# Kernel tuning notes

Hardware: AMD Instinct MI355X
Metric: run time of the kernel (lower is better)

## Reference

```python
import jax, jax.numpy as jnp
import numpy as np

B, T, H = 128, 1024, 200
IN0, OUT = 8, 4  # GRU layer-0 input size (4 targets + 4 emotion), fc output dim


def setup_inputs() -> dict:
    key = jax.random.key(0)
    ks = jax.random.split(key, 12)
    s = 1.0 / np.sqrt(H)  # torch RNN default init: U(-1/sqrt(H), 1/sqrt(H))
    u = lambda k, shp: jax.random.uniform(k, shp, jnp.float32, -s, s)
    return {
        "x": jax.random.normal(ks[0], (B, T, IN0), jnp.float32),
        "W_ih0": u(ks[1], (3 * H, IN0)),
        "W_hh0": u(ks[2], (3 * H, H)),
        "b_ih0": u(ks[3], (3 * H,)),
        "b_hh0": u(ks[4], (3 * H,)),
        "W_ih1": u(ks[5], (3 * H, H)),
        "W_hh1": u(ks[6], (3 * H, H)),
        "b_ih1": u(ks[7], (3 * H,)),
        "b_hh1": u(ks[8], (3 * H,)),
        "W_fc": u(ks[9], (OUT, H)),
        "b_fc": u(ks[10], (OUT,)),
        "xlens": jax.random.randint(ks[11], (B,), 1, T + 1),
    }


def _gru_cell(h, gx, W_hh, b_hh):
    # torch GRU cell: gx = W_ih @ x + b_ih precomputed, gates order [r, z, n]
    gh = h @ W_hh.T + b_hh
    ir, iz, i_n = jnp.split(gx, 3, axis=-1)
    hr, hz, hn = jnp.split(gh, 3, axis=-1)
    r = jax.nn.sigmoid(ir + hr)
    z = jax.nn.sigmoid(iz + hz)
    n = jnp.tanh(i_n + r * hn)
    return (1.0 - z) * n + z * h


def _forward(x, W_ih0, W_hh0, b_ih0, b_hh0, W_ih1, W_hh1, b_ih1, b_hh1, W_fc, b_fc):
    b, t, _ = x.shape
    emotion = x[:, 0, -4:]                      # (B,4) frozen at t=0, as in source
    targets = x[:, :, :4]                       # (B,T,4)
    # step inputs: t=0 -> ones(B,4); t>0 -> targets[:, t-1] (teacher forcing)
    tf = jnp.concatenate([jnp.ones((b, 1, 4), x.dtype), targets[:, :-1, :]], axis=1)
    inputs = jnp.concatenate(
        [tf, jnp.broadcast_to(emotion[:, None, :], (b, t, 4))], axis=-1)  # (B,T,8)
    # precompute layer-0 input projections for all steps (one big GEMM)
    gx0 = jnp.einsum("btc,gc->btg", inputs, W_ih0) + b_ih0  # (B,T,3H)

    def step(carry, gx0_t):
        h0, h1 = carry
        h0 = _gru_cell(h0, gx0_t, W_hh0, b_hh0)
        gx1 = h0 @ W_ih1.T + b_ih1
        h1 = _gru_cell(h1, gx1, W_hh1, b_hh1)
        out = jnp.tanh(h1 @ W_fc.T + b_fc)      # fused fc + tanh
        return (h0, h1), out

    h0 = jnp.zeros((b, H), x.dtype)
    h1 = jnp.zeros((b, H), x.dtype)
    _, outs = jax.lax.scan(step, (h0, h1), jnp.swapaxes(gx0, 0, 1))  # (T,B,4)
    return jnp.swapaxes(outs, 0, 1)             # (B,T,4)


def reference(x, W_ih0, W_hh0, b_ih0, b_hh0, W_ih1, W_hh1, b_ih1, b_hh1, W_fc, b_fc, xlens):
    # xlens is accepted but unused, exactly as in the source forward()
    return _forward(x, W_ih0, W_hh0, b_ih0, b_hh0, W_ih1, W_hh1, b_ih1, b_hh1, W_fc, b_fc)
```

## Files before the change

kernel.cpp:

```cpp
#include <hip/hip_runtime.h>
#include <hip/hip_bf16.h>


#define TT 1024
#define HH 200
#define NB 16
#define HS 13
#define KP 232

typedef __attribute__((ext_vector_type(8))) short short8;
typedef __attribute__((ext_vector_type(4))) float f32x4;

__device__ __forceinline__ float sigm(float v) { return 1.0f / (1.0f + __expf(-v)); }
__device__ __forceinline__ float tanh_fast(float v) {
  float e = __expf(-2.0f * v);
  return (1.0f - e) / (1.0f + e);
}
__device__ __forceinline__ uint llc_load_u32(const uint* p) {
  return __hip_atomic_load(p, __ATOMIC_RELAXED, __HIP_MEMORY_SCOPE_SYSTEM);
}
__device__ __forceinline__ void llc_store_u32(uint* p, uint v) {
  __hip_atomic_store(p, v, __ATOMIC_RELAXED, __HIP_MEMORY_SCOPE_SYSTEM);
}
__device__ __forceinline__ float bfu2f(ushort u) {
  return __uint_as_float(((uint)u) << 16);
}
__device__ __forceinline__ ushort f2bfu(float f) {
  __hip_bfloat16 b = __float2bfloat16(f);
  return *(ushort*)&b;
}
__device__ __forceinline__ uint packf(float h) {
  ushort hi = f2bfu(h);
  float  fh = bfu2f(hi);
  ushort lo = f2bfu(h - fh);
  return (uint)hi | ((uint)lo << 16);
}

__global__ __launch_bounds__(256, 1) void gru2_mfma(
    const float* __restrict__ x,
    const float* __restrict__ Wih0, const float* __restrict__ Whh0,
    const float* __restrict__ bih0, const float* __restrict__ bhh0,
    const float* __restrict__ Wih1, const float* __restrict__ Whh1,
    const float* __restrict__ bih1, const float* __restrict__ bhh1,
    const float* __restrict__ Wfc,  const float* __restrict__ bfc,
    float* __restrict__ out,
    uint* __restrict__ h0g, uint* __restrict__ h1g, int* __restrict__ bars)
{
  __shared__ __align__(16) ushort hBh[2][NB][KP];
  __shared__ __align__(16) ushort hBl[2][NB][KP];
  __shared__ float D[117][17];
  __shared__ float Wi0[39][8];
  __shared__ float bi0[39], bh0[39], bi1[39], bh1[39], bfs[4];
  __shared__ float xc[NB][8];

  const int tid  = threadIdx.x;
  const int wave = tid >> 6;
  const int lane = tid & 63;
  const int m15  = lane & 15;
  const int q    = lane >> 4;

  const int g  = blockIdx.x & 7;
  const int s  = blockIdx.x >> 3;
  const int b0 = g * NB;
  const int j0 = s * HS;
  const int hs = (HH - j0 < HS) ? (HH - j0) : HS;
  const int th   = 3 * hs;
  const int h0r  = 6 * hs;
  const int T0   = (h0r + 15) >> 4;
  const int NT   = T0 + ((th + 15) >> 4);
  const bool isOut = (s == 15);

  short8 Ah[2][7], Al[2][7];
  #pragma unroll
  for (int mt = 0; mt < 2; ++mt) {
    const int T = wave * 2 + mt;
    const bool fc  = isOut && (wave == 2) && (mt == 0);
    const bool val = fc || (T < NT);
    #pragma unroll
    for (int kt = 0; kt < 7; ++kt) {
      short8 vh = {0,0,0,0,0,0,0,0}, vl = {0,0,0,0,0,0,0,0};
      #pragma unroll
      for (int j = 0; j < 8; ++j) {
        const int k = kt * 32 + q * 8 + j;
        float w = 0.0f;
        if (val && k < HH) {
          if (fc) {
            if (m15 < 4) w = Wfc[m15 * HH + k];
          } else {
            const int p = T * 16 + m15;
            int r = -1;
            if (p < h0r) r = p;
            else if (p >= T0 * 16 && (p - T0 * 16) < th) r = h0r + (p - T0 * 16);
            if (r >= 0) {
              const int m  = r / th, rr = r - m * th;
              const int qq = rr / hs, jj = rr - qq * hs;
              const float* src = (m == 0) ? Whh0 : ((m == 1) ? Wih1 : Whh1);
              w = src[(qq * HH + j0 + jj) * HH + k];
            }
          }
        }
        const ushort uh = f2bfu(w);
        const ushort ul = f2bfu(w - bfu2f(uh));
        vh[j] = (short)uh; vl[j] = (short)ul;
      }
      Ah[mt][kt] = vh; Al[mt][kt] = vl;
    }
  }

  for (int u = tid; u < th * 8; u += 256) {
    int rr = u >> 3, c = u & 7;
    int qq = rr / hs, jj = rr - qq * hs;
    Wi0[rr][c] = Wih0[(qq * HH + j0 + jj) * 8 + c];
  }
  for (int u = tid; u < th; u += 256) {
    int qq = u / hs, jj = u - qq * hs;
    int grow = qq * HH + j0 + jj;
    bi0[u] = bih0[grow]; bh0[u] = bhh0[grow];
    bi1[u] = bih1[grow]; bh1[u] = bhh1[grow];
  }
  if (tid < 4) bfs[tid] = bfc[tid];
  for (int u = tid; u < 2 * NB * KP / 2; u += 256) ((uint*)hBh)[u] = 0;
  for (int u = tid; u < 2 * NB * KP / 2; u += 256) ((uint*)hBl)[u] = 0;
  __syncthreads();

  int* bar = &bars[g * 64];
  const int cj = tid >> 4, cb = tid & 15;

  for (int t = 0; t <= TT + 1; ++t) {
    const uint* h0src = h0g + ((t + 1) & 1) * (128 * HH);
    const uint* h1src = h1g + (t & 1) * (128 * HH);
    uint tmp[25];
    #pragma unroll
    for (int i = 0; i < 25; ++i) {
      const int u  = tid + i * 256;
      const int st = u / 3200, rem = u - st * 3200;
      const int b  = rem / 200, k = rem - b * 200;
      tmp[i] = llc_load_u32(&(st ? h1src : h0src)[(b0 + b) * HH + k]);
    }
    #pragma unroll
    for (int i = 0; i < 25; ++i) {
      const int u  = tid + i * 256;
      const int st = u / 3200, rem = u - st * 3200;
      const int b  = rem / 200, k = rem - b * 200;
      hBh[st][b][k] = (ushort)(tmp[i] & 0xffff);
      hBl[st][b][k] = (ushort)(tmp[i] >> 16);
    }
    if (tid < 128 && t < TT) {
      int b = tid >> 3, c = tid & 7;
      float v;
      if (c < 4) v = (t == 0) ? 1.0f : x[((b0 + b) * TT + (t - 1)) * 8 + c];
      else       v = x[(b0 + b) * TT * 8 + c];
      xc[b][c] = v;
    }
    __syncthreads();

    #pragma unroll
    for (int mt = 0; mt < 2; ++mt) {
      const int T = wave * 2 + mt;
      const bool fc  = isOut && (wave == 2) && (mt == 0);
      const bool val = fc || (T < NT);
      if (!val) continue;
      const int st = fc ? 1 : ((T < T0) ? 0 : 1);
      const ushort* Bh = &hBh[st][m15][0];
      const ushort* Bl = &hBl[st][m15][0];
      f32x4 acc = {0.f, 0.f, 0.f, 0.f};
      #pragma unroll
      for (int kt = 0; kt < 7; ++kt) {
        const short8 bh = *(const short8*)&Bh[kt * 32 + q * 8];
        const short8 bl = *(const short8*)&Bl[kt * 32 + q * 8];
        acc = __builtin_amdgcn_mfma_f32_16x16x32_bf16(Ah[mt][kt], bh, acc, 0, 0, 0);
        acc = __builtin_amdgcn_mfma_f32_16x16x32_bf16(Ah[mt][kt], bl, acc, 0, 0, 0);
        acc = __builtin_amdgcn_mfma_f32_16x16x32_bf16(Al[mt][kt], bh, acc, 0, 0, 0);
      }
      if (fc) {
        if (t >= 2) {
          #pragma unroll
          for (int i = 0; i < 4; ++i) {
            const int p = q * 4 + i;
            if (p < 4)
              out[((b0 + m15) * TT + (t - 2)) * 4 + p] = tanh_fast(acc[i] + bfs[p]);
          }
        }
      } else {
        #pragma unroll
        for (int i = 0; i < 4; ++i) {
          const int p = T * 16 + q * 4 + i;
          int r = -1;
          if (p < h0r) r = p;
          else if (p >= T0 * 16 && (p - T0 * 16) < th) r = h0r + (p - T0 * 16);
          if (r >= 0) D[r][m15] = acc[i];
        }
      }
    }
    __syncthreads();

    if (cj < hs) {
      const float hv0 = bfu2f(hBh[0][cb][j0 + cj]) + bfu2f(hBl[0][cb][j0 + cj]);
      const float hv1 = bfu2f(hBh[1][cb][j0 + cj]) + bfu2f(hBl[1][cb][j0 + cj]);
      if (t < TT) {
        float ir = bi0[cj], iz = bi0[hs + cj], in_ = bi0[2 * hs + cj];
        #pragma unroll
        for (int c = 0; c < 8; ++c) {
          const float xv = xc[cb][c];
          ir  += Wi0[cj][c] * xv;
          iz  += Wi0[hs + cj][c] * xv;
          in_ += Wi0[2 * hs + cj][c] * xv;
        }
        const float hr = D[cj][cb] + bh0[cj];
        const float hz = D[hs + cj][cb] + bh0[hs + cj];
        const float hn = D[2 * hs + cj][cb] + bh0[2 * hs + cj];
        const float r = sigm(ir + hr), z = sigm(iz + hz);
        const float n = tanh_fast(in_ + r * hn);
        llc_store_u32(&h0g[(t & 1) * (128 * HH) + (b0 + cb) * HH + j0 + cj],
                      packf((1.0f - z) * n + z * hv0));
      }
      if (t >= 1 && t <= TT) {
        const float ir  = D[3 * hs + cj][cb] + bi1[cj];
        const float iz  = D[4 * hs + cj][cb] + bi1[hs + cj];
        const float in_ = D[5 * hs + cj][cb] + bi1[2 * hs + cj];
        const float hr  = D[6 * hs + cj][cb] + bh1[cj];
        const float hz  = D[7 * hs + cj][cb] + bh1[hs + cj];
        const float hn  = D[8 * hs + cj][cb] + bh1[2 * hs + cj];
        const float r = sigm(ir + hr), z = sigm(iz + hz);
        const float n = tanh_fast(in_ + r * hn);
        llc_store_u32(&h1g[((t + 1) & 1) * (128 * HH) + (b0 + cb) * HH + j0 + cj],
                      packf((1.0f - z) * n + z * hv1));
      }
    }

    __syncthreads();
    if (tid == 0) {
      __hip_atomic_fetch_add(bar, 1, __ATOMIC_RELAXED, __HIP_MEMORY_SCOPE_SYSTEM);
      const int target = 16 * (t + 1);
      while (__hip_atomic_load(bar, __ATOMIC_RELAXED, __HIP_MEMORY_SCOPE_SYSTEM) < target)
        __builtin_amdgcn_s_sleep(1);
    }
    __syncthreads();
  }
}

extern "C" void kernel_launch(void* const* d_in, const int* in_sizes, int n_in,
                              void* d_out, int out_size, void* d_ws, size_t ws_size,
                              hipStream_t stream) {
  uint* ws = (uint*)d_ws;
  hipMemsetAsync(d_ws, 0, (size_t)(102400 + 512) * sizeof(uint), stream);
  gru2_mfma<<<128, 256, 0, stream>>>(
      (const float*)d_in[0],
      (const float*)d_in[1], (const float*)d_in[2],
      (const float*)d_in[3], (const float*)d_in[4],
      (const float*)d_in[5], (const float*)d_in[6],
      (const float*)d_in[7], (const float*)d_in[8],
      (const float*)d_in[9], (const float*)d_in[10],
      (float*)d_out, ws, ws + 51200, (int*)(ws + 102400));
}
```

Measured before the change: 3.170 ms.

## Replace atomic counter barrier with per-block flags and MFMA-fragment LDS layout

The shared atomic counter barrier (one fetch_add plus spin per block per step) is replaced by per-block step flags. Each block writes its own flag and wave 0 polls all 16 flags in its group with a wave vote. The hidden-state staging in LDS is changed to a fragment-major layout so each lane reads its MFMA B operand with one contiguous 16-byte load per k-tile. Both tiles of a wave now share the same B loads. This aims to cut barrier contention and LDS read overhead on the serial recurrence, at the cost of relying on relaxed flag ordering for correctness.

```diff
diff --git a/kernel.cpp b/kernel.cpp
--- a/kernel.cpp
+++ b/kernel.cpp
@@ -2,11 +2,12 @@
 #include <hip/hip_bf16.h>
 
 
-#define TT 1024
-#define HH 200
-#define NB 16
-#define HS 13
-#define KP 232
+#define TT   1024
+#define HH   200
+#define NB   16
+#define HS   13
+#define HBUF 25600
+#define PST  3584
 
 typedef __attribute__((ext_vector_type(8))) short short8;
 typedef __attribute__((ext_vector_type(4))) float f32x4;
@@ -22,21 +23,18 @@
 __device__ __forceinline__ void llc_store_u32(uint* p, uint v) {
   __hip_atomic_store(p, v, __ATOMIC_RELAXED, __HIP_MEMORY_SCOPE_SYSTEM);
 }
-__device__ __forceinline__ float bfu2f(ushort u) {
-  return __uint_as_float(((uint)u) << 16);
-}
+__device__ __forceinline__ float bfu2f(ushort u) { return __uint_as_float(((uint)u) << 16); }
 __device__ __forceinline__ ushort f2bfu(float f) {
   __hip_bfloat16 b = __float2bfloat16(f);
   return *(ushort*)&b;
 }
 __device__ __forceinline__ uint packf(float h) {
   ushort hi = f2bfu(h);
-  float  fh = bfu2f(hi);
-  ushort lo = f2bfu(h - fh);
-  return (uint)hi | ((uint)lo << 16);
-}
-
-__global__ __launch_bounds__(256, 1) void gru2_mfma(
+  ushort lo = f2bfu(h - bfu2f(hi));
+  return (uint)hi | (((uint)lo) << 16);
+}
+
+__global__ __launch_bounds__(256, 1) void gru2_frag(
     const float* __restrict__ x,
     const float* __restrict__ Wih0, const float* __restrict__ Whh0,
     const float* __restrict__ bih0, const float* __restrict__ bhh0,
@@ -44,10 +42,10 @@
     const float* __restrict__ bih1, const float* __restrict__ bhh1,
     const float* __restrict__ Wfc,  const float* __restrict__ bfc,
     float* __restrict__ out,
-    uint* __restrict__ h0g, uint* __restrict__ h1g, int* __restrict__ bars)
+    uint* __restrict__ h0g, uint* __restrict__ h1g, uint* __restrict__ flags)
 {
-  __shared__ __align__(16) ushort hBh[2][NB][KP];
-  __shared__ __align__(16) ushort hBl[2][NB][KP];
+  __shared__ __align__(16) ushort hFh[2 * PST];
+  __shared__ __align__(16) ushort hFl[2 * PST];
   __shared__ float D[117][17];
   __shared__ float Wi0[39][8];
   __shared__ float bi0[39], bh0[39], bi1[39], bh1[39], bfs[4];
@@ -64,139 +62,188 @@
   const int b0 = g * NB;
   const int j0 = s * HS;
   const int hs = (HH - j0 < HS) ? (HH - j0) : HS;
-  const int th   = 3 * hs;
-  const int h0r  = 6 * hs;
-  const int T0   = (h0r + 15) >> 4;
-  const int NT   = T0 + ((th + 15) >> 4);
+  const int th  = 3 * hs;
+  const int h0r = 6 * hs;
+  const int T0  = (h0r + 15) >> 4;
+  const int NT  = T0 + ((th + 15) >> 4);
   const bool isOut = (s == 15);
 
   short8 Ah[2][7], Al[2][7];
   #pragma unroll
-  for (int mt = 0; mt < 2; ++mt) {
-    const int T = wave * 2 + mt;
-    const bool fc  = isOut && (wave == 2) && (mt == 0);
-    const bool val = fc || (T < NT);
+  for (int tt = 0; tt < 2; ++tt) {
+    const int T = 2 * wave + tt;
+    const bool isFC = isOut && (T == NT);
+    const bool val  = (T < NT) || isFC;
     #pragma unroll
     for (int kt = 0; kt < 7; ++kt) {
       short8 vh = {0,0,0,0,0,0,0,0}, vl = {0,0,0,0,0,0,0,0};
-      #pragma unroll
-      for (int j = 0; j < 8; ++j) {
-        const int k = kt * 32 + q * 8 + j;
-        float w = 0.0f;
-        if (val && k < HH) {
-          if (fc) {
-            if (m15 < 4) w = Wfc[m15 * HH + k];
-          } else {
-            const int p = T * 16 + m15;
-            int r = -1;
-            if (p < h0r) r = p;
-            else if (p >= T0 * 16 && (p - T0 * 16) < th) r = h0r + (p - T0 * 16);
-            if (r >= 0) {
-              const int m  = r / th, rr = r - m * th;
-              const int qq = rr / hs, jj = rr - qq * hs;
-              const float* src = (m == 0) ? Whh0 : ((m == 1) ? Wih1 : Whh1);
-              w = src[(qq * HH + j0 + jj) * HH + k];
+      if (val) {
+        #pragma unroll
+        for (int j = 0; j < 8; ++j) {
+          const int k = kt * 32 + q * 8 + j;
+          float w = 0.0f;
+          if (k < HH) {
+            if (isFC) {
+              if (m15 < 4) w = Wfc[m15 * HH + k];
+            } else {
+              const int p = T * 16 + m15;
+              int r = -1;
+              if (p < h0r) r = p;
+              else { const int pp = p - T0 * 16; if (pp >= 0 && pp < th) r = h0r + pp; }
+              if (r >= 0) {
+                const int m = r / th, rr = r - m * th;
+                const int q3 = rr / hs, jj = rr - q3 * hs;
+                const float* src = (m == 0) ? Whh0 : ((m == 1) ? Wih1 : Whh1);
+                w = src[(q3 * HH + j0 + jj) * HH + k];
+              }
             }
           }
-        }
-        const ushort uh = f2bfu(w);
-        const ushort ul = f2bfu(w - bfu2f(uh));
-        vh[j] = (short)uh; vl[j] = (short)ul;
-      }
-      Ah[mt][kt] = vh; Al[mt][kt] = vl;
-    }
-  }
-
+          const ushort hi = f2bfu(w);
+          const ushort lo = f2bfu(w - bfu2f(hi));
+          vh[j] = (short)hi; vl[j] = (short)lo;
+        }
+      }
+      Ah[tt][kt] = vh; Al[tt][kt] = vl;
+    }
+  }
+
+  for (int u = tid; u < 2 * PST; u += 256) { hFh[u] = 0; hFl[u] = 0; }
   for (int u = tid; u < th * 8; u += 256) {
-    int rr = u >> 3, c = u & 7;
-    int qq = rr / hs, jj = rr - qq * hs;
-    Wi0[rr][c] = Wih0[(qq * HH + j0 + jj) * 8 + c];
+    const int rr = u >> 3, c = u & 7;
+    const int q3 = rr / hs, jj = rr - q3 * hs;
+    Wi0[rr][c] = Wih0[(q3 * HH + j0 + jj) * 8 + c];
   }
   for (int u = tid; u < th; u += 256) {
-    int qq = u / hs, jj = u - qq * hs;
-    int grow = qq * HH + j0 + jj;
+    const int q3 = u / hs, jj = u - q3 * hs;
+    const int grow = q3 * HH + j0 + jj;
     bi0[u] = bih0[grow]; bh0[u] = bhh0[grow];
     bi1[u] = bih1[grow]; bh1[u] = bhh1[grow];
   }
   if (tid < 4) bfs[tid] = bfc[tid];
-  for (int u = tid; u < 2 * NB * KP / 2; u += 256) ((uint*)hBh)[u] = 0;
-  for (int u = tid; u < 2 * NB * KP / 2; u += 256) ((uint*)hBl)[u] = 0;
+
+  int boff[25], lofs[25]; uint stm = 0;
+  #pragma unroll
+  for (int i = 0; i < 25; ++i) {
+    const int u  = tid + i * 256;
+    const int b  = u & 15;
+    const int v2 = u >> 4;
+    const int st = (v2 >= 200) ? 1 : 0;
+    const int k  = v2 - st * 200;
+    const int kt = k >> 5, r32 = k & 31, qq = r32 >> 3, j = r32 & 7;
+    boff[i] = (b0 + b) * HH + k;
+    lofs[i] = st * PST + kt * 512 + (b + 16 * qq) * 8 + j;
+    if (st) stm |= (1u << i);
+  }
+
+  const int cj = tid >> 4, cb = tid & 15;
+  const bool gAct = (cj < hs);
+  int hvix = 0;
+  if (gAct) {
+    const int k = j0 + cj;
+    const int kt = k >> 5, r32 = k & 31, qq = r32 >> 3, j = r32 & 7;
+    hvix = kt * 512 + (cb + 16 * qq) * 8 + j;
+  }
+
+  uint* const flg = flags + g * 32;
   __syncthreads();
 
-  int* bar = &bars[g * 64];
-  const int cj = tid >> 4, cb = tid & 15;
-
   for (int t = 0; t <= TT + 1; ++t) {
-    const uint* h0src = h0g + ((t + 1) & 1) * (128 * HH);
-    const uint* h1src = h1g + (t & 1) * (128 * HH);
-    uint tmp[25];
-    #pragma unroll
-    for (int i = 0; i < 25; ++i) {
-      const int u  = tid + i * 256;
-      const int st = u / 3200, rem = u - st * 3200;
-      const int b  = rem / 200, k = rem - b * 200;
-      tmp[i] = llc_load_u32(&(st ? h1src : h0src)[(b0 + b) * HH + k]);
-    }
-    #pragma unroll
-    for (int i = 0; i < 25; ++i) {
-      const int u  = tid + i * 256;
-      const int st = u / 3200, rem = u - st * 3200;
-      const int b  = rem / 200, k = rem - b * 200;
-      hBh[st][b][k] = (ushort)(tmp[i] & 0xffff);
-      hBl[st][b][k] = (ushort)(tmp[i] >> 16);
-    }
     if (tid < 128 && t < TT) {
-      int b = tid >> 3, c = tid & 7;
+      const int b = tid >> 3, c = tid & 7;
       float v;
       if (c < 4) v = (t == 0) ? 1.0f : x[((b0 + b) * TT + (t - 1)) * 8 + c];
       else       v = x[(b0 + b) * TT * 8 + c];
       xc[b][c] = v;
     }
-    __syncthreads();
-
+
+    if (wave == 0) {
+      const uint tgt = (uint)t;
+      for (;;) {
+        const uint f = (lane < 16) ? llc_load_u32(flg + lane) : tgt;
+        if (__all((int)(f >= tgt))) break;
+        __builtin_amdgcn_s_sleep(2);
+      }
+    }
+    __syncthreads();
+
+    const uint* h0s = h0g + ((t + 1) & 1) * HBUF;
+    const uint* h1s = h1g + (t & 1) * HBUF;
+    uint v[25];
     #pragma unroll
-    for (int mt = 0; mt < 2; ++mt) {
-      const int T = wave * 2 + mt;
-      const bool fc  = isOut && (wave == 2) && (mt == 0);
-      const bool val = fc || (T < NT);
-      if (!val) continue;
-      const int st = fc ? 1 : ((T < T0) ? 0 : 1);
-      const ushort* Bh = &hBh[st][m15][0];
-      const ushort* Bl = &hBl[st][m15][0];
-      f32x4 acc = {0.f, 0.f, 0.f, 0.f};
+    for (int i = 0; i < 25; ++i)
+      v[i] = llc_load_u32((((stm >> i) & 1) ? h1s : h0s) + boff[i]);
+    #pragma unroll
+    for (int i = 0; i < 25; ++i) {
+      hFh[lofs[i]] = (ushort)(v[i] & 0xffffu);
+      hFl[lofs[i]] = (ushort)(v[i] >> 16);
+    }
+    __syncthreads();
+
+    {
+      const int  Ta = 2 * wave, Tb = Ta + 1;
+      const bool fa = isOut && (Ta == NT);
+      const bool fb = isOut && (Tb == NT);
+      const bool va = (Ta < NT) || fa, vb = (Tb < NT) || fb;
+      const int  sa = (fa || Ta >= T0) ? 1 : 0;
+      const int  sb = (fb || Tb >= T0) ? 1 : 0;
+      f32x4 acc0 = {0.f,0.f,0.f,0.f}, acc1 = {0.f,0.f,0.f,0.f};
+      const int lb = lane * 8;
       #pragma unroll
-      for (int kt = 0; kt < 7; ++kt) {
-        const short8 bh = *(const short8*)&Bh[kt * 32 + q * 8];
-        const short8 bl = *(const short8*)&Bl[kt * 32 + q * 8];
-        acc = __builtin_amdgcn_mfma_f32_16x16x32_bf16(Ah[mt][kt], bh, acc, 0, 0, 0);
-        acc = __builtin_amdgcn_mfma_f32_16x16x32_bf16(Ah[mt][kt], bl, acc, 0, 0, 0);
-        acc = __builtin_amdgcn_mfma_f32_16x16x32_bf16(Al[mt][kt], bh, acc, 0, 0, 0);
-      }
-      if (fc) {
-        if (t >= 2) {
-          #pragma unroll
-          for (int i = 0; i < 4; ++i) {
-            const int p = q * 4 + i;
-            if (p < 4)
-              out[((b0 + m15) * TT + (t - 2)) * 4 + p] = tanh_fast(acc[i] + bfs[p]);
+      for (int st = 0; st < 2; ++st) {
+        const bool nA = va && (sa == st), nB = vb && (sb == st);
+        if (!(nA || nB)) continue;
+        const ushort* bh = hFh + st * PST + lb;
+        const ushort* bl = hFl + st * PST + lb;
+        #pragma unroll
+        for (int kt = 0; kt < 7; ++kt) {
+          const short8 Bh = *(const short8*)(bh + kt * 512);
+          const short8 Bl = *(const short8*)(bl + kt * 512);
+          if (nA) {
+            acc0 = __builtin_amdgcn_mfma_f32_16x16x32_bf16(Ah[0][kt], Bh, acc0, 0, 0, 0);
+            acc0 = __builtin_amdgcn_mfma_f32_16x16x32_bf16(Ah[0][kt], Bl, acc0, 0, 0, 0);
+            acc0 = __builtin_amdgcn_mfma_f32_16x16x32_bf16(Al[0][kt], Bh, acc0, 0, 0, 0);
           }
-        }
-      } else {
+          if (nB) {
+            acc1 = __builtin_amdgcn_mfma_f32_16x16x32_bf16(Ah[1][kt], Bh, acc1, 0, 0, 0);
+            acc1 = __builtin_amdgcn_mfma_f32_16x16x32_bf16(Ah[1][kt], Bl, acc1, 0, 0, 0);
+            acc1 = __builtin_amdgcn_mfma_f32_16x16x32_bf16(Al[1][kt], Bh, acc1, 0, 0, 0);
+          }
+        }
+      }
+      if (va && !fa) {
         #pragma unroll
         for (int i = 0; i < 4; ++i) {
-          const int p = T * 16 + q * 4 + i;
+          const int p = Ta * 16 + q * 4 + i;
           int r = -1;
           if (p < h0r) r = p;
-          else if (p >= T0 * 16 && (p - T0 * 16) < th) r = h0r + (p - T0 * 16);
-          if (r >= 0) D[r][m15] = acc[i];
-        }
-      }
-    }
-    __syncthreads();
-
-    if (cj < hs) {
-      const float hv0 = bfu2f(hBh[0][cb][j0 + cj]) + bfu2f(hBl[0][cb][j0 + cj]);
-      const float hv1 = bfu2f(hBh[1][cb][j0 + cj]) + bfu2f(hBl[1][cb][j0 + cj]);
+          else { const int pp = p - T0 * 16; if (pp >= 0 && pp < th) r = h0r + pp; }
+          if (r >= 0) D[r][m15] = acc0[i];
+        }
+      }
+      if (vb && !fb) {
+        #pragma unroll
+        for (int i = 0; i < 4; ++i) {
+          const int p = Tb * 16 + q * 4 + i;
+          int r = -1;
+          if (p < h0r) r = p;
+          else { const int pp = p - T0 * 16; if (pp >= 0 && pp < th) r = h0r + pp; }
+          if (r >= 0) D[r][m15] = acc1[i];
+        }
+      }
+      if (fb && t >= 2) {
+        #pragma unroll
+        for (int i = 0; i < 4; ++i) {
+          const int p = q * 4 + i;
+          if (p < 4)
+            out[((b0 + m15) * TT + (t - 2)) * 4 + p] = tanh_fast(acc1[i] + bfs[p]);
+        }
+      }
+    }
+    __syncthreads();
+
+    if (gAct) {
+      const float hv0 = bfu2f(hFh[hvix]) + bfu2f(hFl[hvix]);
+      const float hv1 = bfu2f(hFh[PST + hvix]) + bfu2f(hFl[PST + hvix]);
       if (t < TT) {
         float ir = bi0[cj], iz = bi0[hs + cj], in_ = bi0[2 * hs + cj];
         #pragma unroll
@@ -211,7 +258,7 @@
         const float hn = D[2 * hs + cj][cb] + bh0[2 * hs + cj];
         const float r = sigm(ir + hr), z = sigm(iz + hz);
         const float n = tanh_fast(in_ + r * hn);
-        llc_store_u32(&h0g[(t & 1) * (128 * HH) + (b0 + cb) * HH + j0 + cj],
+        llc_store_u32(h0g + (t & 1) * HBUF + (b0 + cb) * HH + (j0 + cj),
                       packf((1.0f - z) * n + z * hv0));
       }
       if (t >= 1 && t <= TT) {
@@ -223,19 +270,13 @@
         const float hn  = D[8 * hs + cj][cb] + bh1[2 * hs + cj];
         const float r = sigm(ir + hr), z = sigm(iz + hz);
         const float n = tanh_fast(in_ + r * hn);
-        llc_store_u32(&h1g[((t + 1) & 1) * (128 * HH) + (b0 + cb) * HH + j0 + cj],
+        llc_store_u32(h1g + ((t + 1) & 1) * HBUF + (b0 + cb) * HH + (j0 + cj),
                       packf((1.0f - z) * n + z * hv1));
       }
     }
 
     __syncthreads();
-    if (tid == 0) {
-      __hip_atomic_fetch_add(bar, 1, __ATOMIC_RELAXED, __HIP_MEMORY_SCOPE_SYSTEM);
-      const int target = 16 * (t + 1);
-      while (__hip_atomic_load(bar, __ATOMIC_RELAXED, __HIP_MEMORY_SCOPE_SYSTEM) < target)
-        __builtin_amdgcn_s_sleep(1);
-    }
-    __syncthreads();
+    if (tid == 0) llc_store_u32(flg + s, (uint)(t + 1));
   }
 }
 
@@ -243,13 +284,13 @@
                               void* d_out, int out_size, void* d_ws, size_t ws_size,
                               hipStream_t stream) {
   uint* ws = (uint*)d_ws;
-  hipMemsetAsync(d_ws, 0, (size_t)(102400 + 512) * sizeof(uint), stream);
-  gru2_mfma<<<128, 256, 0, stream>>>(
+  hipMemsetAsync(d_ws, 0, (size_t)(4 * HBUF + 256) * sizeof(uint), stream);
+  gru2_frag<<<128, 256, 0, stream>>>(
       (const float*)d_in[0],
       (const float*)d_in[1], (const float*)d_in[2],
       (const float*)d_in[3], (const float*)d_in[4],
       (const float*)d_in[5], (const float*)d_in[6],
       (const float*)d_in[7], (const float*)d_in[8],
       (const float*)d_in[9], (const float*)d_in[10],
-      (float*)d_out, ws, ws + 51200, (int*)(ws + 102400));
-}
+      (float*)d_out, ws, ws + 2 * HBUF, ws + 4 * HBUF);
+}
```

Result: slower. 5.777 ms (+82.2%).
